# Kernel tuning notes

Hardware: AMD Instinct MI355X
Metric: run time of the kernel (lower is better)

Reference implementation:

```python
import jax, jax.numpy as jnp
import numpy as np

N_G, N_U, E, C = 100000, 100000, 3200000, 2000000


def graph_conv(x, edges, W_rel, W_root, b):
    # PyG GraphConv (aggr='add'): out_i = (sum_{j->i} x_j) @ W_rel + x_i @ W_root + b
    src, dst = edges[0], edges[1]
    agg = jax.ops.segment_sum(x[src], dst, num_segments=x.shape[0])
    return agg @ W_rel + x @ W_root + b


def setup_inputs() -> dict:
    key = jax.random.key(0)
    ks = jax.random.split(key, 16)
    d = {
        'x_u': jax.random.normal(ks[0], (N_U, 4), jnp.float32),
        'x_g': jax.random.normal(ks[1], (N_G, 4), jnp.float32),
        'candidates': jax.random.randint(ks[2], (C, 2), 0, N_G + N_U, jnp.int64),
        'edges': jax.random.randint(ks[3], (2, E), 0, N_G, jnp.int64),
        # GraphConv(4,8)
        'W1_rel': jax.random.normal(ks[4], (4, 8), jnp.float32) * 0.5,
        'W1_root': jax.random.normal(ks[5], (4, 8), jnp.float32) * 0.5,
        'b1': jax.random.normal(ks[6], (8,), jnp.float32) * 0.1,
        # GraphConv(8,16)
        'W2_rel': jax.random.normal(ks[7], (8, 16), jnp.float32) * 0.35,
        'W2_root': jax.random.normal(ks[8], (8, 16), jnp.float32) * 0.35,
        'b2': jax.random.normal(ks[9], (16,), jnp.float32) * 0.1,
        # fc_unconnected: Linear(4,16) (Dropout is identity in eval)
        'W_un': jax.random.normal(ks[10], (4, 16), jnp.float32) * 0.5,
        'b_un': jax.random.normal(ks[11], (16,), jnp.float32) * 0.1,
        # fc: Linear(32,64) -> SELU -> Linear(64,1)
        'W_fc1': jax.random.normal(ks[12], (32, 64), jnp.float32) * 0.18,
        'b_fc1': jax.random.normal(ks[13], (64,), jnp.float32) * 0.1,
        'W_fc2': jax.random.normal(ks[14], (64, 1), jnp.float32) * 0.12,
        'b_fc2': jax.random.normal(ks[15], (1,), jnp.float32) * 0.1,
    }
    return d


def reference(x_u, x_g, candidates, edges,
              W1_rel, W1_root, b1, W2_rel, W2_root, b2,
              W_un, b_un, W_fc1, b_fc1, W_fc2, b_fc2):
    x_unconnected = x_u @ W_un + b_un                      # [N_u, 16]
    h = jax.nn.selu(graph_conv(x_g, edges, W1_rel, W1_root, b1))   # [N_g, 8]
    x_graph = jax.nn.selu(graph_conv(h, edges, W2_rel, W2_root, b2))  # [N_g, 16]
    x_stacked = jnp.concatenate([x_graph, x_unconnected], axis=0)  # [N_g+N_u, 16]
    ec = jnp.concatenate([x_stacked[candidates[:, 0]],
                          x_stacked[candidates[:, 1]]], axis=1)    # [C, 32]
    hidden = jax.nn.selu(ec @ W_fc1 + b_fc1)               # [C, 64]
    out = (hidden @ W_fc2 + b_fc2).squeeze(-1)             # [C]
    return out


if __name__ == '__main__':
    print(reference(**setup_inputs()).shape)
```

## Files before the change

### kernel.cpp

```cpp
#include <hip/hip_runtime.h>
#include <hip/hip_bf16.h>

#define NG 100000
#define NU 100000
#define NE 3200000
#define NC 2000000

#define BSZ 128
#define NBK 782
#define CAP 5120
#define B1CH 4096

typedef __attribute__((ext_vector_type(8))) short short8;
typedef __attribute__((ext_vector_type(4))) float floatx4;
typedef unsigned short ushortx8 __attribute__((ext_vector_type(8)));

__device__ __forceinline__ float selu_f(float x) {
    const float LAM = 1.0507009873554805f;
    const float ALA = 1.7580993408473766f;
    const float L2E = 1.44269504088896340736f;
    float e = __builtin_amdgcn_exp2f(fminf(x, 0.f) * L2E);
    return fmaf(LAM, fmaxf(x, 0.f), fmaf(ALA, e, -ALA));
}

__device__ __forceinline__ float bfbits2f(unsigned short u) {
    return __uint_as_float(((unsigned)u) << 16);
}

__device__ __forceinline__ unsigned short f2bfbits(float f) {
    union { __hip_bfloat16 h; unsigned short u; } cv;
    cv.h = __float2bfloat16(f);
    return cv.u;
}

__device__ __forceinline__ float ldf(const void* p, int i, int isbf) {
    return isbf ? bfbits2f(((const unsigned short*)p)[i]) : ((const float*)p)[i];
}

__global__ __launch_bounds__(256) void k_bin1(const void* __restrict__ edges,
        int* __restrict__ gcur, unsigned int* __restrict__ glist) {
    __shared__ unsigned int tmp[B1CH];
    __shared__ unsigned short tfid[B1CH];
    __shared__ unsigned int ord[B1CH];
    __shared__ unsigned short osid[B1CH];
    __shared__ int hist[NBK];
    __shared__ int lstart[NBK];
    __shared__ int gbase[NBK];
    __shared__ int ofs[NBK];
    __shared__ int wsum[4];
    __shared__ int se64;

    int tid = threadIdx.x;
    long long base = (long long)blockIdx.x * B1CH;
    int chunk = (int)(NE - base);
    if (chunk > B1CH) chunk = B1CH;

    if (tid < 64) {
        unsigned long long m3 =
            __ballot(((const unsigned int*)edges)[2 * tid + 1] == 0u);
        if (tid == 0) se64 = (__popcll(m3) >= 48) ? 1 : 0;
    }
    for (int b = tid; b < NBK; b += 256) hist[b] = 0;
    __syncthreads();
    int e64 = se64;

    for (int i = 0; i < B1CH / 512; ++i) {
        int idx = i * 512 + tid * 2;
        if (idx < chunk) {
            int s0, s1, d0, d1;
            if (e64) {
                const long long* el = (const long long*)edges;
                longlong2 sv = *(const longlong2*)(el + base + idx);
                longlong2 dv = *(const longlong2*)(el + NE + base + idx);
                s0 = (int)sv.x; s1 = (int)sv.y;
                d0 = (int)dv.x; d1 = (int)dv.y;
            } else {
                const int* ei = (const int*)edges;
                int2 sv = *(const int2*)(ei + base + idx);
                int2 dv = *(const int2*)(ei + NE + base + idx);
                s0 = sv.x; s1 = sv.y; d0 = dv.x; d1 = dv.y;
            }
            int f0 = d0 >> 7;
            tmp[idx] = ((unsigned)s0 << 7) | (unsigned)(d0 & 127);
            tfid[idx] = (unsigned short)f0;
            atomicAdd(&hist[f0], 1);
            if (idx + 1 < chunk) {
                int f1 = d1 >> 7;
                tmp[idx + 1] = ((unsigned)s1 << 7) | (unsigned)(d1 & 127);
                tfid[idx + 1] = (unsigned short)f1;
                atomicAdd(&hist[f1], 1);
            }
        }
    }
    __syncthreads();

    {
        int s0 = tid * 4;
        int loc[4];
        int ssum = 0;
#pragma unroll
        for (int j = 0; j < 4; ++j) {
            int b = s0 + j;
            int c = (b < NBK) ? hist[b] : 0;
            loc[j] = ssum;
            ssum += c;
        }
        int lane = tid & 63, w = tid >> 6;
        int inc = ssum;
#pragma unroll
        for (int off = 1; off < 64; off <<= 1) {
            int v = __shfl_up(inc, off, 64);
            if (lane >= off) inc += v;
        }
        if (lane == 63) wsum[w] = inc;
        __syncthreads();
        int wbase = 0;
        for (int k = 0; k < 4; ++k)
            if (k < w) wbase += wsum[k];
        int excl = wbase + inc - ssum;
#pragma unroll
        for (int j = 0; j < 4; ++j) {
            int b = s0 + j;
            if (b < NBK) lstart[b] = excl + loc[j];
        }
    }
    __syncthreads();

    for (int b = tid; b < NBK; b += 256) {
        int c = hist[b];
        gbase[b] = (c > 0) ? atomicAdd(&gcur[b], c) : 0;
        ofs[b] = lstart[b];
    }
    __syncthreads();

    for (int i = 0; i < B1CH / 256; ++i) {
        int idx = i * 256 + tid;
        if (idx < chunk) {
            int f = tfid[idx];
            int pos = atomicAdd(&ofs[f], 1);
            ord[pos] = tmp[idx];
            osid[pos] = (unsigned short)f;
        }
    }
    __syncthreads();

    for (int i = 0; i < B1CH / 256; ++i) {
        int idx = i * 256 + tid;
        if (idx < chunk) {
            int f = osid[idx];
            int p = gbase[f] + (idx - lstart[f]);
            if (p < CAP) glist[(long long)f * CAP + p] = ord[idx];
        }
    }
}

__global__ __launch_bounds__(256) void k_sort(const int* __restrict__ gcur,
        unsigned int* __restrict__ glist,
        int* __restrict__ dstoff, int* __restrict__ ddeg,
        const unsigned int* __restrict__ xw, const unsigned int* __restrict__ cw,
        const unsigned int* __restrict__ ew, int* __restrict__ flags) {
    __shared__ unsigned int tmp[CAP];
    __shared__ int hist[BSZ];
    __shared__ int cur[BSZ];
    __shared__ int wtot;
    int b = blockIdx.x;
    int tid = threadIdx.x;

    if (b == 0 && tid < 64) {
        unsigned lo = xw[tid] & 0xffffu;
        unsigned e = (lo >> 7) & 0xff;
        unsigned long long m1 = __ballot(e >= 112 && e <= 134);
        unsigned long long m2 = __ballot(cw[2 * tid + 1] == 0u);
        unsigned long long m3 = __ballot(ew[2 * tid + 1] == 0u);
        if (tid == 0) {
            flags[0] = (__popcll(m1) >= 32) ? 1 : 0;
            flags[1] = (__popcll(m2) >= 48) ? 1 : 0;
            flags[2] = (__popcll(m3) >= 48) ? 1 : 0;
        }
    }

    int cnt = gcur[b];
    if (cnt > CAP) cnt = CAP;
    unsigned int* lp = glist + (long long)b * CAP;

    if (tid < BSZ) hist[tid] = 0;
    __syncthreads();
    for (int k = tid; k < cnt; k += 256) {
        unsigned u = lp[k];
        tmp[k] = u;
        atomicAdd(&hist[u & 127], 1);
    }
    __syncthreads();
    int h = (tid < BSZ) ? hist[tid] : 0;
    int s = h;
#pragma unroll
    for (int off = 1; off < 64; off <<= 1) {
        int v = __shfl_up(s, off, 64);
        if ((tid & 63) >= off) s += v;
    }
    if (tid == 63) wtot = s;
    __syncthreads();
    if (tid >= 64 && tid < BSZ) s += wtot;
    if (tid < BSZ) {
        int excl = s - h;
        cur[tid] = excl;
        int d = b * BSZ + tid;
        if (d < NG) {
            dstoff[d] = b * CAP + excl;
            ddeg[d] = h;
        }
    }
    __syncthreads();
    for (int k = tid; k < cnt; k += 256) {
        unsigned u = tmp[k];
        int pos = atomicAdd(&cur[u & 127], 1);
        lp[pos] = u >> 7;
    }
}

__global__ __launch_bounds__(256) void k_gather1(const int* __restrict__ dstoff,
        const int* __restrict__ ddeg, const unsigned int* __restrict__ glist,
        const void* __restrict__ xg,
        const void* __restrict__ W1r, const void* __restrict__ W1o,
        const void* __restrict__ b1, unsigned short* __restrict__ hbf,
        const int* __restrict__ flags) {
    int gid = blockIdx.x * 256 + threadIdx.x;
    int d = gid >> 4;
    if (d >= NG) return;
    int q = gid & 15;
    int isbf = flags[0];
    int start = dstoff[d];
    int deg = ddeg[d];
    float a0 = 0.f, a1 = 0.f, a2 = 0.f, a3 = 0.f;
    if (isbf) {
        const unsigned short* xp = (const unsigned short*)xg;
        int k = q;
        for (; k + 16 < deg; k += 32) {
            int s0 = glist[start + k];
            int s1 = glist[start + k + 16];
            ushort4 r0 = *(const ushort4*)(xp + s0 * 4);
            ushort4 r1 = *(const ushort4*)(xp + s1 * 4);
            a0 += bfbits2f(r0.x) + bfbits2f(r1.x);
            a1 += bfbits2f(r0.y) + bfbits2f(r1.y);
            a2 += bfbits2f(r0.z) + bfbits2f(r1.z);
            a3 += bfbits2f(r0.w) + bfbits2f(r1.w);
        }
        for (; k < deg; k += 16) {
            int s = glist[start + k];
            ushort4 r = *(const ushort4*)(xp + s * 4);
            a0 += bfbits2f(r.x); a1 += bfbits2f(r.y);
            a2 += bfbits2f(r.z); a3 += bfbits2f(r.w);
        }
    } else {
        const float* xp = (const float*)xg;
        int k = q;
        for (; k + 16 < deg; k += 32) {
            int s0 = glist[start + k];
            int s1 = glist[start + k + 16];
            float4 r0 = *(const float4*)(xp + s0 * 4);
            float4 r1 = *(const float4*)(xp + s1 * 4);
            a0 += r0.x + r1.x;
            a1 += r0.y + r1.y;
            a2 += r0.z + r1.z;
            a3 += r0.w + r1.w;
        }
        for (; k < deg; k += 16) {
            int s = glist[start + k];
            float4 r = *(const float4*)(xp + s * 4);
            a0 += r.x; a1 += r.y; a2 += r.z; a3 += r.w;
        }
    }
#pragma unroll
    for (int off = 1; off < 16; off <<= 1) {
        a0 += __shfl_xor(a0, off);
        a1 += __shfl_xor(a1, off);
        a2 += __shfl_xor(a2, off);
        a3 += __shfl_xor(a3, off);
    }
    if (q < 8) {
        float a[4] = {a0, a1, a2, a3};
        float v = ldf(b1, q, isbf);
#pragma unroll
        for (int c = 0; c < 4; ++c)
            v += a[c] * ldf(W1r, c * 8 + q, isbf)
               + ldf(xg, d * 4 + c, isbf) * ldf(W1o, c * 8 + q, isbf);
        hbf[d * 8 + q] = f2bfbits(selu_f(v));
    }
}

#define G2BLK ((16 * NG + 255) / 256)
#define UCBLK ((NU + 255) / 256)

__global__ __launch_bounds__(256) void k_gather2(const int* __restrict__ dstoff,
        const int* __restrict__ ddeg, const unsigned int* __restrict__ glist,
        const ushortx8* __restrict__ hbf,
        const void* __restrict__ W2r, const void* __restrict__ W2o,
        const void* __restrict__ b2, unsigned short* __restrict__ xs,
        const void* __restrict__ xu, const void* __restrict__ Wun,
        const void* __restrict__ bun, const int* __restrict__ flags) {
    int isbf = flags[0];
    if (blockIdx.x >= G2BLK) {
        int u = (blockIdx.x - G2BLK) * 256 + threadIdx.x;
        if (u >= NU) return;
        float x[4];
#pragma unroll
        for (int k = 0; k < 4; ++k) x[k] = ldf(xu, u * 4 + k, isbf);
        ushortx8 lo, hi;
#pragma unroll
        for (int j = 0; j < 16; ++j) {
            float v = ldf(bun, j, isbf);
#pragma unroll
            for (int k = 0; k < 4; ++k)
                v += x[k] * ldf(Wun, k * 16 + j, isbf);
            unsigned short bb = f2bfbits(v);
            if (j < 8) lo[j] = bb; else hi[j - 8] = bb;
        }
        ushortx8* xp = (ushortx8*)(xs + (NG + u) * 16);
        xp[0] = lo;
        xp[1] = hi;
        return;
    }
    int gid = blockIdx.x * 256 + threadIdx.x;
    int d = gid >> 4;
    if (d >= NG) return;
    int q = gid & 15;
    int start = dstoff[d];
    int deg = ddeg[d];
    float a[8] = {0.f, 0.f, 0.f, 0.f, 0.f, 0.f, 0.f, 0.f};
    int k = q;
    for (; k + 16 < deg; k += 32) {
        int s0 = glist[start + k];
        int s1 = glist[start + k + 16];
        ushortx8 r0 = hbf[s0];
        ushortx8 r1 = hbf[s1];
#pragma unroll
        for (int c = 0; c < 8; ++c)
            a[c] += bfbits2f((unsigned short)r0[c]) + bfbits2f((unsigned short)r1[c]);
    }
    for (; k < deg; k += 16) {
        int s = glist[start + k];
        ushortx8 r = hbf[s];
#pragma unroll
        for (int c = 0; c < 8; ++c) a[c] += bfbits2f((unsigned short)r[c]);
    }
#pragma unroll
    for (int off = 1; off < 16; off <<= 1) {
#pragma unroll
        for (int c = 0; c < 8; ++c) a[c] += __shfl_xor(a[c], off);
    }
    ushortx8 hr = hbf[d];
    float hv[8];
#pragma unroll
    for (int c = 0; c < 8; ++c) hv[c] = bfbits2f((unsigned short)hr[c]);
    float v = ldf(b2, q, isbf);
#pragma unroll
    for (int c = 0; c < 8; ++c)
        v += a[c] * ldf(W2r, c * 16 + q, isbf)
           + hv[c] * ldf(W2o, c * 16 + q, isbf);
    xs[d * 16 + q] = f2bfbits(selu_f(v));
}

__device__ __forceinline__ int ld_candrow(const void* cand, int c, int hp, int c64) {
    const int* ci = (const int*)cand;
    return c64 ? ci[(2 * c + hp) * 2] : ci[2 * c + hp];
}

__global__ __launch_bounds__(256, 5) void k_fc(const unsigned short* __restrict__ xs,
        const void* __restrict__ cand,
        const void* __restrict__ Wfc1, const void* __restrict__ bfc1,
        const void* __restrict__ Wfc2, const void* __restrict__ bfc2,
        void* __restrict__ out, const int* __restrict__ flags,
        int t0, int t1) {
    const float LAM = 1.0507009873554805f;
    const float ALA = 1.7580993408473766f;
    const float L2E = 1.44269504088896340736f;
    const float AR2 = 1.6732632423543772f * 1.44269504088896340736f;
    const float SCL = 1.0507009873554805f / 1.44269504088896340736f;
    int lane = threadIdx.x & 63;
    int wid = (blockIdx.x * blockDim.x + threadIdx.x) >> 6;
    int m = lane & 15;
    int half = lane >> 4;
    int isbf = flags[0], c64 = flags[1];

    short8 wfrag[4];
    floatx4 cbias[4];
    float w2s[4][4];
    float c_corr;
    if (isbf) {
        const unsigned short* W1p = (const unsigned short*)Wfc1;
#pragma unroll
        for (int t = 0; t < 4; ++t)
#pragma unroll
            for (int j = 0; j < 8; ++j)
                wfrag[t][j] = (short)f2bfbits(
                    bfbits2f(W1p[(half * 8 + j) * 64 + t * 16 + m]) * L2E);
        const unsigned short* b1p = (const unsigned short*)bfc1;
        const unsigned short* w2p = (const unsigned short*)Wfc2;
        float asum = 0.f;
#pragma unroll
        for (int t = 0; t < 4; ++t)
#pragma unroll
            for (int r = 0; r < 4; ++r) {
                int h = t * 16 + half * 4 + r;
                cbias[t][r] = bfbits2f(b1p[h]) * L2E;
                float w2 = bfbits2f(w2p[h]);
                w2s[t][r] = w2 * SCL;
                asum += w2 * ALA;
            }
        asum += __shfl_xor(asum, 16, 64);
        asum += __shfl_xor(asum, 32, 64);
        c_corr = bfbits2f(((const unsigned short*)bfc2)[0]) - asum;
    } else {
        const float* W1p = (const float*)Wfc1;
#pragma unroll
        for (int t = 0; t < 4; ++t)
#pragma unroll
            for (int j = 0; j < 8; ++j)
                wfrag[t][j] = (short)f2bfbits(
                    W1p[(half * 8 + j) * 64 + t * 16 + m] * L2E);
        const float* b1p = (const float*)bfc1;
        const float* w2p = (const float*)Wfc2;
        float asum = 0.f;
#pragma unroll
        for (int t = 0; t < 4; ++t)
#pragma unroll
            for (int r = 0; r < 4; ++r) {
                int h = t * 16 + half * 4 + r;
                cbias[t][r] = b1p[h] * L2E;
                float w2 = w2p[h];
                w2s[t][r] = w2 * SCL;
                asum += w2 * ALA;
            }
        asum += __shfl_xor(asum, 16, 64);
        asum += __shfl_xor(asum, 32, 64);
        c_corr = ((const float*)bfc2)[0] - asum;
    }

    int nW = (gridDim.x * blockDim.x) >> 6;
    if (t0 + wid >= t1) return;
    int tw = t0 + wid;

    int half1 = half & 1;
    int hp = half >> 1;
    int q1 = tw + nW, q2 = tw + 2 * nW, q3 = tw + 3 * nW, q4 = tw + 4 * nW;
    int r0i = ld_candrow(cand, tw * 16 + m, hp, c64);
    int r1i = ld_candrow(cand, ((q1 < t1) ? q1 : tw) * 16 + m, hp, c64);
    int r2i = ld_candrow(cand, ((q2 < t1) ? q2 : tw) * 16 + m, hp, c64);
    int r3i = ld_candrow(cand, ((q3 < t1) ? q3 : tw) * 16 + m, hp, c64);
    int r4i = ld_candrow(cand, ((q4 < t1) ? q4 : tw) * 16 + m, hp, c64);
    {
        short8 af0 = *(const short8*)(xs + r0i * 16 + half1 * 8);
        short8 af1 = *(const short8*)(xs + r1i * 16 + half1 * 8);
        short8 af2 = *(const short8*)(xs + r2i * 16 + half1 * 8);
        short8 af3 = *(const short8*)(xs + r3i * 16 + half1 * 8);

#pragma unroll 2
        for (int t = tw; t < t1; t += nW) {
            int tn5 = t + 5 * nW;
            int r5i = ld_candrow(cand, ((tn5 < t1) ? tn5 : t) * 16 + m, hp, c64);
            short8 af4 = *(const short8*)(xs + r4i * 16 + half1 * 8);

            float ps[4];
#pragma unroll
            for (int tt = 0; tt < 4; ++tt) {
                floatx4 ac = __builtin_amdgcn_mfma_f32_16x16x32_bf16(
                    wfrag[tt], af0, cbias[tt], 0, 0, 0);
                float s = 0.f;
#pragma unroll
                for (int r = 0; r < 4; ++r) {
                    float v = ac[r];
                    float mx = fmaxf(v, 0.f);
                    float e = __builtin_amdgcn_exp2f(fminf(v, 0.f));
                    s = fmaf(w2s[tt][r], fmaf(AR2, e, mx), s);
                }
                ps[tt] = s;
            }
            float part = (ps[0] + ps[1]) + (ps[2] + ps[3]);
            part += __shfl_xor(part, 16, 64);
            part += __shfl_xor(part, 32, 64);
            if (half == 0) {
                float o = part + c_corr;
                if (isbf) ((unsigned short*)out)[t * 16 + m] = f2bfbits(o);
                else ((float*)out)[t * 16 + m] = o;
            }
            af0 = af1;
            af1 = af2;
            af2 = af3;
            af3 = af4;
            r4i = r5i;
        }
    }
}

extern "C" void kernel_launch(void* const* d_in, const int* in_sizes, int n_in,
                              void* d_out, int out_size, void* d_ws, size_t ws_size,
                              hipStream_t stream) {
    const void* x_u = d_in[0];
    const void* x_g = d_in[1];
    const void* cand = d_in[2];
    const void* edges = d_in[3];
    const void* W1r = d_in[4];
    const void* W1o = d_in[5];
    const void* b1 = d_in[6];
    const void* W2r = d_in[7];
    const void* W2o = d_in[8];
    const void* b2 = d_in[9];
    const void* Wun = d_in[10];
    const void* bun = d_in[11];
    const void* Wfc1 = d_in[12];
    const void* bfc1 = d_in[13];
    const void* Wfc2 = d_in[14];
    const void* bfc2 = d_in[15];

    char* ws = (char*)d_ws;
    int* flags = (int*)ws;
    int* gcur = (int*)(ws + 64);
    unsigned int* glist = (unsigned int*)(ws + 4160);
    size_t glist_bytes = (size_t)NBK * CAP * 4;
    char* p = ws + 4160 + glist_bytes;
    int* dstoff = (int*)p;
    int* ddeg = (int*)(p + 400000);
    unsigned short* hbf = (unsigned short*)(p + 800000);
    unsigned short* xs = (unsigned short*)(p + 2400000);

    hipMemsetAsync(gcur, 0, 3200, stream);

    k_bin1<<<(NE + B1CH - 1) / B1CH, 256, 0, stream>>>(edges, gcur, glist);
    k_sort<<<NBK, 256, 0, stream>>>(gcur, glist, dstoff, ddeg,
                                    (const unsigned int*)x_u,
                                    (const unsigned int*)cand,
                                    (const unsigned int*)edges, flags);
    k_gather1<<<(16 * NG + 255) / 256, 256, 0, stream>>>(dstoff, ddeg, glist, x_g,
                                                         W1r, W1o, b1, hbf, flags);
    k_gather2<<<G2BLK + UCBLK, 256, 0, stream>>>(dstoff, ddeg, glist,
                                                 (const ushortx8*)hbf,
                                                 W2r, W2o, b2, xs,
                                                 x_u, Wun, bun, flags);
    const int nTiles = NC / 16;
    const int tMid = nTiles / 2;
    k_fc<<<1280, 256, 0, stream>>>(xs, cand, Wfc1, bfc1, Wfc2, bfc2, d_out, flags,
                                   0, tMid);
    k_fc<<<1280, 256, 0, stream>>>(xs, cand, Wfc1, bfc1, Wfc2, bfc2, d_out, flags,
                                   tMid, nTiles);
}
```

Before: 253.1 us.

## Drop per-destination sort; aggregate bucketed edges with LDS float atomics

The per-bucket counting sort kernel is removed. Both gather kernels now process one 128-destination bucket per block, reading the unsorted packed (src, local dst) list and accumulating neighbour features into shared memory with float atomicAdd, then computing the GraphConv output per destination. The dtype-detection flags move into k_bin1. This saves a kernel launch and a full read/write pass over the edge list, at the cost of LDS atomic contention and a summation order that is no longer deterministic.

After: 445.2 us. +75.9%, slower.

```diff
diff --git a/kernel.cpp b/kernel.cpp
--- a/kernel.cpp
+++ b/kernel.cpp
@@ -38,7 +38,9 @@
 }
 
 __global__ __launch_bounds__(256) void k_bin1(const void* __restrict__ edges,
-        int* __restrict__ gcur, unsigned int* __restrict__ glist) {
+        int* __restrict__ gcur, unsigned int* __restrict__ glist,
+        const unsigned int* __restrict__ xw, const unsigned int* __restrict__ cw,
+        int* __restrict__ flags) {
     __shared__ unsigned int tmp[B1CH];
     __shared__ unsigned short tfid[B1CH];
     __shared__ unsigned int ord[B1CH];
@@ -59,6 +61,17 @@
         unsigned long long m3 =
             __ballot(((const unsigned int*)edges)[2 * tid + 1] == 0u);
         if (tid == 0) se64 = (__popcll(m3) >= 48) ? 1 : 0;
+        if (blockIdx.x == 0) {
+            unsigned lo = xw[tid] & 0xffffu;
+            unsigned e = (lo >> 7) & 0xff;
+            unsigned long long m1 = __ballot(e >= 112 && e <= 134);
+            unsigned long long m2 = __ballot(cw[2 * tid + 1] == 0u);
+            if (tid == 0) {
+                flags[0] = (__popcll(m1) >= 32) ? 1 : 0;
+                flags[1] = (__popcll(m2) >= 48) ? 1 : 0;
+                flags[2] = (__popcll(m3) >= 48) ? 1 : 0;
+            }
+        }
     }
     for (int b = tid; b < NBK; b += 256) hist[b] = 0;
     __syncthreads();
@@ -154,153 +167,107 @@
     }
 }
 
-__global__ __launch_bounds__(256) void k_sort(const int* __restrict__ gcur,
-        unsigned int* __restrict__ glist,
-        int* __restrict__ dstoff, int* __restrict__ ddeg,
-        const unsigned int* __restrict__ xw, const unsigned int* __restrict__ cw,
-        const unsigned int* __restrict__ ew, int* __restrict__ flags) {
-    __shared__ unsigned int tmp[CAP];
-    __shared__ int hist[BSZ];
-    __shared__ int cur[BSZ];
-    __shared__ int wtot;
-    int b = blockIdx.x;
-    int tid = threadIdx.x;
-
-    if (b == 0 && tid < 64) {
-        unsigned lo = xw[tid] & 0xffffu;
-        unsigned e = (lo >> 7) & 0xff;
-        unsigned long long m1 = __ballot(e >= 112 && e <= 134);
-        unsigned long long m2 = __ballot(cw[2 * tid + 1] == 0u);
-        unsigned long long m3 = __ballot(ew[2 * tid + 1] == 0u);
-        if (tid == 0) {
-            flags[0] = (__popcll(m1) >= 32) ? 1 : 0;
-            flags[1] = (__popcll(m2) >= 48) ? 1 : 0;
-            flags[2] = (__popcll(m3) >= 48) ? 1 : 0;
-        }
-    }
-
-    int cnt = gcur[b];
-    if (cnt > CAP) cnt = CAP;
-    unsigned int* lp = glist + (long long)b * CAP;
-
-    if (tid < BSZ) hist[tid] = 0;
-    __syncthreads();
-    for (int k = tid; k < cnt; k += 256) {
-        unsigned u = lp[k];
-        tmp[k] = u;
-        atomicAdd(&hist[u & 127], 1);
-    }
-    __syncthreads();
-    int h = (tid < BSZ) ? hist[tid] : 0;
-    int s = h;
-#pragma unroll
-    for (int off = 1; off < 64; off <<= 1) {
-        int v = __shfl_up(s, off, 64);
-        if ((tid & 63) >= off) s += v;
-    }
-    if (tid == 63) wtot = s;
-    __syncthreads();
-    if (tid >= 64 && tid < BSZ) s += wtot;
-    if (tid < BSZ) {
-        int excl = s - h;
-        cur[tid] = excl;
-        int d = b * BSZ + tid;
-        if (d < NG) {
-            dstoff[d] = b * CAP + excl;
-            ddeg[d] = h;
-        }
-    }
-    __syncthreads();
-    for (int k = tid; k < cnt; k += 256) {
-        unsigned u = tmp[k];
-        int pos = atomicAdd(&cur[u & 127], 1);
-        lp[pos] = u >> 7;
-    }
-}
-
-__global__ __launch_bounds__(256) void k_gather1(const int* __restrict__ dstoff,
-        const int* __restrict__ ddeg, const unsigned int* __restrict__ glist,
-        const void* __restrict__ xg,
+__global__ __launch_bounds__(256) void k_gather1(const int* __restrict__ gcur,
+        const unsigned int* __restrict__ glist, const void* __restrict__ xg,
         const void* __restrict__ W1r, const void* __restrict__ W1o,
         const void* __restrict__ b1, unsigned short* __restrict__ hbf,
         const int* __restrict__ flags) {
-    int gid = blockIdx.x * 256 + threadIdx.x;
-    int d = gid >> 4;
-    if (d >= NG) return;
-    int q = gid & 15;
+    __shared__ float acc[BSZ][4];
+    int b = blockIdx.x;
+    int tid = threadIdx.x;
     int isbf = flags[0];
-    int start = dstoff[d];
-    int deg = ddeg[d];
-    float a0 = 0.f, a1 = 0.f, a2 = 0.f, a3 = 0.f;
+    int cnt = gcur[b];
+    if (cnt > CAP) cnt = CAP;
+    const unsigned int* lp = glist + (long long)b * CAP;
+
+    float* pa = &acc[0][0];
+    for (int i = tid; i < BSZ * 4; i += 256) pa[i] = 0.f;
+    __syncthreads();
+
     if (isbf) {
         const unsigned short* xp = (const unsigned short*)xg;
-        int k = q;
-        for (; k + 16 < deg; k += 32) {
-            int s0 = glist[start + k];
-            int s1 = glist[start + k + 16];
-            ushort4 r0 = *(const ushort4*)(xp + s0 * 4);
-            ushort4 r1 = *(const ushort4*)(xp + s1 * 4);
-            a0 += bfbits2f(r0.x) + bfbits2f(r1.x);
-            a1 += bfbits2f(r0.y) + bfbits2f(r1.y);
-            a2 += bfbits2f(r0.z) + bfbits2f(r1.z);
-            a3 += bfbits2f(r0.w) + bfbits2f(r1.w);
-        }
-        for (; k < deg; k += 16) {
-            int s = glist[start + k];
+        for (int k = tid; k < cnt; k += 256) {
+            unsigned u = lp[k];
+            int s = (int)(u >> 7), dl = (int)(u & 127);
             ushort4 r = *(const ushort4*)(xp + s * 4);
-            a0 += bfbits2f(r.x); a1 += bfbits2f(r.y);
-            a2 += bfbits2f(r.z); a3 += bfbits2f(r.w);
+            atomicAdd(&acc[dl][0], bfbits2f(r.x));
+            atomicAdd(&acc[dl][1], bfbits2f(r.y));
+            atomicAdd(&acc[dl][2], bfbits2f(r.z));
+            atomicAdd(&acc[dl][3], bfbits2f(r.w));
         }
     } else {
         const float* xp = (const float*)xg;
-        int k = q;
-        for (; k + 16 < deg; k += 32) {
-            int s0 = glist[start + k];
-            int s1 = glist[start + k + 16];
-            float4 r0 = *(const float4*)(xp + s0 * 4);
-            float4 r1 = *(const float4*)(xp + s1 * 4);
-            a0 += r0.x + r1.x;
-            a1 += r0.y + r1.y;
-            a2 += r0.z + r1.z;
-            a3 += r0.w + r1.w;
-        }
-        for (; k < deg; k += 16) {
-            int s = glist[start + k];
+        for (int k = tid; k < cnt; k += 256) {
+            unsigned u = lp[k];
+            int s = (int)(u >> 7), dl = (int)(u & 127);
             float4 r = *(const float4*)(xp + s * 4);
-            a0 += r.x; a1 += r.y; a2 += r.z; a3 += r.w;
-        }
-    }
-#pragma unroll
-    for (int off = 1; off < 16; off <<= 1) {
-        a0 += __shfl_xor(a0, off);
-        a1 += __shfl_xor(a1, off);
-        a2 += __shfl_xor(a2, off);
-        a3 += __shfl_xor(a3, off);
-    }
-    if (q < 8) {
-        float a[4] = {a0, a1, a2, a3};
-        float v = ldf(b1, q, isbf);
-#pragma unroll
-        for (int c = 0; c < 4; ++c)
-            v += a[c] * ldf(W1r, c * 8 + q, isbf)
-               + ldf(xg, d * 4 + c, isbf) * ldf(W1o, c * 8 + q, isbf);
-        hbf[d * 8 + q] = f2bfbits(selu_f(v));
-    }
-}
-
-#define G2BLK ((16 * NG + 255) / 256)
+            atomicAdd(&acc[dl][0], r.x);
+            atomicAdd(&acc[dl][1], r.y);
+            atomicAdd(&acc[dl][2], r.z);
+            atomicAdd(&acc[dl][3], r.w);
+        }
+    }
+    __syncthreads();
+
+    int dl = tid >> 1;
+    int d = b * BSZ + dl;
+    if (d >= NG) return;
+    int q0 = (tid & 1) * 4;
+    float a0 = acc[dl][0], a1 = acc[dl][1], a2 = acc[dl][2], a3 = acc[dl][3];
+    float o[4];
+    if (isbf) {
+        const unsigned short* xp = (const unsigned short*)xg;
+        const unsigned short* wr = (const unsigned short*)W1r;
+        const unsigned short* wo = (const unsigned short*)W1o;
+        const unsigned short* bp = (const unsigned short*)b1;
+        float x0 = bfbits2f(xp[d * 4 + 0]), x1 = bfbits2f(xp[d * 4 + 1]);
+        float x2 = bfbits2f(xp[d * 4 + 2]), x3 = bfbits2f(xp[d * 4 + 3]);
+#pragma unroll
+        for (int j = 0; j < 4; ++j) {
+            int q = q0 + j;
+            float v = bfbits2f(bp[q]);
+            v += a0 * bfbits2f(wr[0 * 8 + q]) + a1 * bfbits2f(wr[1 * 8 + q])
+               + a2 * bfbits2f(wr[2 * 8 + q]) + a3 * bfbits2f(wr[3 * 8 + q]);
+            v += x0 * bfbits2f(wo[0 * 8 + q]) + x1 * bfbits2f(wo[1 * 8 + q])
+               + x2 * bfbits2f(wo[2 * 8 + q]) + x3 * bfbits2f(wo[3 * 8 + q]);
+            o[j] = selu_f(v);
+        }
+    } else {
+        const float* xp = (const float*)xg;
+        const float* wr = (const float*)W1r;
+        const float* wo = (const float*)W1o;
+        const float* bp = (const float*)b1;
+        float x0 = xp[d * 4 + 0], x1 = xp[d * 4 + 1];
+        float x2 = xp[d * 4 + 2], x3 = xp[d * 4 + 3];
+#pragma unroll
+        for (int j = 0; j < 4; ++j) {
+            int q = q0 + j;
+            float v = bp[q];
+            v += a0 * wr[0 * 8 + q] + a1 * wr[1 * 8 + q]
+               + a2 * wr[2 * 8 + q] + a3 * wr[3 * 8 + q];
+            v += x0 * wo[0 * 8 + q] + x1 * wo[1 * 8 + q]
+               + x2 * wo[2 * 8 + q] + x3 * wo[3 * 8 + q];
+            o[j] = selu_f(v);
+        }
+    }
+    ushort4 w;
+    w.x = f2bfbits(o[0]); w.y = f2bfbits(o[1]);
+    w.z = f2bfbits(o[2]); w.w = f2bfbits(o[3]);
+    *(ushort4*)(hbf + d * 8 + q0) = w;
+}
+
 #define UCBLK ((NU + 255) / 256)
 
-__global__ __launch_bounds__(256) void k_gather2(const int* __restrict__ dstoff,
-        const int* __restrict__ ddeg, const unsigned int* __restrict__ glist,
-        const ushortx8* __restrict__ hbf,
+__global__ __launch_bounds__(256) void k_gather2(const int* __restrict__ gcur,
+        const unsigned int* __restrict__ glist, const ushortx8* __restrict__ hbf,
         const void* __restrict__ W2r, const void* __restrict__ W2o,
         const void* __restrict__ b2, unsigned short* __restrict__ xs,
         const void* __restrict__ xu, const void* __restrict__ Wun,
         const void* __restrict__ bun, const int* __restrict__ flags) {
     int isbf = flags[0];
-    if (blockIdx.x >= G2BLK) {
-        int u = (blockIdx.x - G2BLK) * 256 + threadIdx.x;
+    int tid = threadIdx.x;
+    if (blockIdx.x >= NBK) {
+        int u = (blockIdx.x - NBK) * 256 + tid;
         if (u >= NU) return;
         float x[4];
 #pragma unroll
@@ -320,44 +287,67 @@
         xp[1] = hi;
         return;
     }
-    int gid = blockIdx.x * 256 + threadIdx.x;
-    int d = gid >> 4;
+    __shared__ float acc[BSZ][8];
+    int b = blockIdx.x;
+    int cnt = gcur[b];
+    if (cnt > CAP) cnt = CAP;
+    const unsigned int* lp = glist + (long long)b * CAP;
+
+    float* pa = &acc[0][0];
+    for (int i = tid; i < BSZ * 8; i += 256) pa[i] = 0.f;
+    __syncthreads();
+
+    for (int k = tid; k < cnt; k += 256) {
+        unsigned u = lp[k];
+        int s = (int)(u >> 7), dl = (int)(u & 127);
+        ushortx8 r = hbf[s];
+#pragma unroll
+        for (int c = 0; c < 8; ++c)
+            atomicAdd(&acc[dl][c], bfbits2f((unsigned short)r[c]));
+    }
+    __syncthreads();
+
+    int dl = tid >> 1;
+    int d = b * BSZ + dl;
     if (d >= NG) return;
-    int q = gid & 15;
-    int start = dstoff[d];
-    int deg = ddeg[d];
-    float a[8] = {0.f, 0.f, 0.f, 0.f, 0.f, 0.f, 0.f, 0.f};
-    int k = q;
-    for (; k + 16 < deg; k += 32) {
-        int s0 = glist[start + k];
-        int s1 = glist[start + k + 16];
-        ushortx8 r0 = hbf[s0];
-        ushortx8 r1 = hbf[s1];
-#pragma unroll
-        for (int c = 0; c < 8; ++c)
-            a[c] += bfbits2f((unsigned short)r0[c]) + bfbits2f((unsigned short)r1[c]);
-    }
-    for (; k < deg; k += 16) {
-        int s = glist[start + k];
-        ushortx8 r = hbf[s];
-#pragma unroll
-        for (int c = 0; c < 8; ++c) a[c] += bfbits2f((unsigned short)r[c]);
-    }
-#pragma unroll
-    for (int off = 1; off < 16; off <<= 1) {
-#pragma unroll
-        for (int c = 0; c < 8; ++c) a[c] += __shfl_xor(a[c], off);
-    }
+    int q0 = (tid & 1) * 8;
+    float av[8];
+#pragma unroll
+    for (int c = 0; c < 8; ++c) av[c] = acc[dl][c];
     ushortx8 hr = hbf[d];
     float hv[8];
 #pragma unroll
     for (int c = 0; c < 8; ++c) hv[c] = bfbits2f((unsigned short)hr[c]);
-    float v = ldf(b2, q, isbf);
-#pragma unroll
-    for (int c = 0; c < 8; ++c)
-        v += a[c] * ldf(W2r, c * 16 + q, isbf)
-           + hv[c] * ldf(W2o, c * 16 + q, isbf);
-    xs[d * 16 + q] = f2bfbits(selu_f(v));
+    ushortx8 w;
+    if (isbf) {
+        const unsigned short* wr = (const unsigned short*)W2r;
+        const unsigned short* wo = (const unsigned short*)W2o;
+        const unsigned short* bp = (const unsigned short*)b2;
+#pragma unroll
+        for (int j = 0; j < 8; ++j) {
+            int q = q0 + j;
+            float v = bfbits2f(bp[q]);
+#pragma unroll
+            for (int c = 0; c < 8; ++c)
+                v += av[c] * bfbits2f(wr[c * 16 + q])
+                   + hv[c] * bfbits2f(wo[c * 16 + q]);
+            w[j] = (short)f2bfbits(selu_f(v));
+        }
+    } else {
+        const float* wr = (const float*)W2r;
+        const float* wo = (const float*)W2o;
+        const float* bp = (const float*)b2;
+#pragma unroll
+        for (int j = 0; j < 8; ++j) {
+            int q = q0 + j;
+            float v = bp[q];
+#pragma unroll
+            for (int c = 0; c < 8; ++c)
+                v += av[c] * wr[c * 16 + q] + hv[c] * wo[c * 16 + q];
+            w[j] = (short)f2bfbits(selu_f(v));
+        }
+    }
+    *(ushortx8*)(xs + d * 16 + q0) = w;
 }
 
 __device__ __forceinline__ int ld_candrow(const void* cand, int c, int hp, int c64) {
@@ -518,24 +508,20 @@
     unsigned int* glist = (unsigned int*)(ws + 4160);
     size_t glist_bytes = (size_t)NBK * CAP * 4;
     char* p = ws + 4160 + glist_bytes;
-    int* dstoff = (int*)p;
-    int* ddeg = (int*)(p + 400000);
-    unsigned short* hbf = (unsigned short*)(p + 800000);
-    unsigned short* xs = (unsigned short*)(p + 2400000);
+    unsigned short* hbf = (unsigned short*)p;
+    unsigned short* xs = (unsigned short*)(p + 1600000);
 
     hipMemsetAsync(gcur, 0, 3200, stream);
 
-    k_bin1<<<(NE + B1CH - 1) / B1CH, 256, 0, stream>>>(edges, gcur, glist);
-    k_sort<<<NBK, 256, 0, stream>>>(gcur, glist, dstoff, ddeg,
-                                    (const unsigned int*)x_u,
-                                    (const unsigned int*)cand,
-                                    (const unsigned int*)edges, flags);
-    k_gather1<<<(16 * NG + 255) / 256, 256, 0, stream>>>(dstoff, ddeg, glist, x_g,
-                                                         W1r, W1o, b1, hbf, flags);
-    k_gather2<<<G2BLK + UCBLK, 256, 0, stream>>>(dstoff, ddeg, glist,
-                                                 (const ushortx8*)hbf,
-                                                 W2r, W2o, b2, xs,
-                                                 x_u, Wun, bun, flags);
+    k_bin1<<<(NE + B1CH - 1) / B1CH, 256, 0, stream>>>(edges, gcur, glist,
+                                                       (const unsigned int*)x_u,
+                                                       (const unsigned int*)cand,
+                                                       flags);
+    k_gather1<<<NBK, 256, 0, stream>>>(gcur, glist, x_g, W1r, W1o, b1, hbf, flags);
+    k_gather2<<<NBK + UCBLK, 256, 0, stream>>>(gcur, glist,
+                                               (const ushortx8*)hbf,
+                                               W2r, W2o, b2, xs,
+                                               x_u, Wun, bun, flags);
     const int nTiles = NC / 16;
     const int tMid = nTiles / 2;
     k_fc<<<1280, 256, 0, stream>>>(xs, cand, Wfc1, bfc1, Wfc2, bfc2, d_out, flags,
```
